# Kernel tuning notes

Hardware: AMD Instinct MI355X
Metric: run time of the kernel (lower is better)

Reference implementation:

```python
import jax, jax.numpy as jnp
import numpy as np

WINDOW = 2  # hardcoded global in the original module


def band_count(seq_len, window=WINDOW):
    """C[a,b] = number of positions i whose local window covers both a and b.
    Windows (from converse_qk): i=0 -> [0, W]; i=1 -> [0, W+1];
    i=seq-2 -> [seq-W-2, seq-1]; i=seq-1 -> [seq-W-1, seq-1]; else [i-W, i+W].
    """
    i = jnp.arange(seq_len)
    lo = jnp.clip(i - window, 0, None)
    hi = jnp.clip(i + window, None, seq_len - 1)
    lo = jnp.where(i == 1, 0, lo)
    hi = jnp.where(i == 1, window + 1, hi)
    lo = jnp.where(i == seq_len - 2, seq_len - window - 2, lo)
    hi = jnp.where(i == seq_len - 2, seq_len - 1, hi)
    a = jnp.arange(seq_len)[None, :]
    M = ((a >= lo[:, None]) & (a <= hi[:, None])).astype(jnp.float32)  # [i, a]
    return M.T @ M  # [seq, seq]


def setup_inputs() -> dict:
    key = jax.random.key(0)
    ks = jax.random.split(key, 12)
    bs, seq, d_model = 2, 2048, 512
    s = 1.0 / np.sqrt(d_model)
    inp = {
        'q': jax.random.normal(ks[0], (bs, seq, d_model), jnp.float32),
        'k': jax.random.normal(ks[1], (bs, seq, d_model), jnp.float32),
        'v': jax.random.normal(ks[2], (bs, seq, d_model), jnp.float32),
        'Wq': jax.random.normal(ks[3], (d_model, d_model), jnp.float32) * s,
        'bq': jnp.zeros((d_model,), jnp.float32),
        'Wk': jax.random.normal(ks[4], (d_model, d_model), jnp.float32) * s,
        'bk': jnp.zeros((d_model,), jnp.float32),
        'Wv': jax.random.normal(ks[5], (d_model, d_model), jnp.float32) * s,
        'bv': jnp.zeros((d_model,), jnp.float32),
        'Wo': jax.random.normal(ks[6], (d_model, d_model), jnp.float32) * s,
        'bo': jnp.zeros((d_model,), jnp.float32),
    }
    return inp


def reference(q, k, v, Wq, bq, Wk, bk, Wv, bv, Wo, bo):
    bs, seq, d_model = q.shape
    heads = 8
    d_k = d_model // heads
    # projections (torch Linear uses x @ W.T + b; here W stored already transposed)
    qh = (q @ Wq + bq).reshape(bs, seq, heads, d_k).transpose(0, 2, 1, 3)
    kh = (k @ Wk + bk).reshape(bs, seq, heads, d_k).transpose(0, 2, 1, 3)
    vh = (v @ Wv + bv).reshape(bs, seq, heads, d_k).transpose(0, 2, 1, 3)
    C = band_count(seq)  # [seq, seq] window-overlap counts
    scores = jnp.einsum('bhqd,bhkd->bhqk', qh, kh) / jnp.sqrt(jnp.float32(d_k))
    scores = scores * C  # banded count-weighted scores; zeros outside band
    attn = jax.nn.softmax(scores, axis=-1)  # full-row softmax, as in original
    out = jnp.einsum('bhqk,bhkd->bhqd', attn, vh)
    concat = out.transpose(0, 2, 1, 3).reshape(bs, seq, d_model)
    return concat @ Wo + bo
```

## Files before the change

kernel.cpp:

```cpp
#include <hip/hip_runtime.h>
#include <hip/hip_bf16.h>

#define SEQ 2048
#define DM  512
#define BS  2
#define NH  8
#define DK  64
#define MROWS (BS * SEQ)
#define GK 64

typedef __attribute__((ext_vector_type(8))) short bf16x8;
typedef __attribute__((ext_vector_type(4))) float f32x4;

__device__ __forceinline__ unsigned short f2bf(float f) {
    unsigned int u = __float_as_uint(f);
    u += 0x7fff + ((u >> 16) & 1);
    return (unsigned short)(u >> 16);
}
__device__ __forceinline__ float bf2f(unsigned short b) {
    return __uint_as_float((unsigned int)b << 16);
}

#define GLDS16(g, l) __builtin_amdgcn_global_load_lds( \
    (const __attribute__((address_space(1))) void*)(g), \
    (__attribute__((address_space(3))) void*)(unsigned int)(unsigned long long)(l), 16, 0, 0)

__global__ __launch_bounds__(256) void prep_w(const float* __restrict__ Wq, const float* __restrict__ Wk,
                                              const float* __restrict__ Wv, const float* __restrict__ Wo,
                                              const float* __restrict__ bv_,
                                              unsigned short* __restrict__ WqT, unsigned short* __restrict__ WkT,
                                              unsigned short* __restrict__ WvT, unsigned short* __restrict__ WoT,
                                              float* __restrict__ vsum)
{
    __shared__ float tile[32][33];
    const int bid = blockIdx.x;
    if (bid == 0) {
        #pragma unroll
        for (int t = 0; t < 4; ++t) {
            const int idx = threadIdx.x * 4 + t;
            vsum[idx] = (float)SEQ * bv_[idx & (DM - 1)];
        }
    }
    const int z = bid >> 8;
    const int tl = bid & 255;
    const float* W = (z == 0) ? Wq : (z == 1) ? Wk : (z == 2) ? Wv : Wo;
    unsigned short* T = (z == 0) ? WqT : (z == 1) ? WkT : (z == 2) ? WvT : WoT;
    const int n0 = (tl & 15) * 32, k0 = (tl >> 4) * 32;
    const int tx = threadIdx.x & 31;
    const int ty = threadIdx.x >> 5;
    #pragma unroll
    for (int r = 0; r < 32; r += 8)
        tile[ty + r][tx] = W[(size_t)(k0 + ty + r) * DM + n0 + tx];
    __syncthreads();
    #pragma unroll
    for (int r = 0; r < 32; r += 8)
        T[(size_t)(n0 + ty + r) * DM + k0 + tx] = f2bf(tile[tx][ty + r]);
}

__global__ __launch_bounds__(256) void gemm_qkv_cvt(const float* __restrict__ q,
                                                    const float* __restrict__ k,
                                                    const float* __restrict__ v,
                                                    const unsigned short* __restrict__ WqT,
                                                    const unsigned short* __restrict__ WkT,
                                                    const unsigned short* __restrict__ WvT,
                                                    const float* __restrict__ bq, const float* __restrict__ bk,
                                                    const float* __restrict__ bvp,
                                                    unsigned short* __restrict__ Qb, unsigned short* __restrict__ Kb,
                                                    unsigned short* __restrict__ Vb, float* __restrict__ vsum)
{
    __shared__ unsigned short S[2][12288];

    const int g = blockIdx.x;
    const int xcd   = g & 7;
    const int n_idx = (g >> 3) & 3;
    const int t_    = g >> 5;
    const int strip = t_ * 8 + xcd;
    const int z     = strip >> 6;
    const int m0    = (strip & 63) * 64;
    const int n0    = n_idx * 128;

    const float* Af; const unsigned short* BT; const float* bias; unsigned short* C; float* vs;
    if (z == 0)      { Af = q; BT = WqT; bias = bq; C = Qb; vs = nullptr; }
    else if (z == 1) { Af = k; BT = WkT; bias = bk; C = Kb; vs = nullptr; }
    else             { Af = v; BT = WvT; bias = bvp; C = Vb; vs = vsum; }

    const int tid  = threadIdx.x;
    const int lane = tid & 63;
    const int wave = tid >> 6;
    const int wm = (wave & 1) * 32;
    const int wn = (wave >> 1) * 64;
    const int l15 = lane & 15;
    const int q8  = (lane >> 4) * 8;

    f32x4 acc[2][4];
    #pragma unroll
    for (int i = 0; i < 2; ++i)
        #pragma unroll
        for (int j = 0; j < 4; ++j)
            acc[i][j] = (f32x4){0.f, 0.f, 0.f, 0.f};

    const int arow = tid >> 4;
    const int akl  = (tid & 15) * 4;
    const int awoff = ((akl >> 5) * 2048) + (akl & 31);
    const float* agp = Af + (size_t)(m0 + arow) * DM + akl;

    const unsigned short* gb[4];
    int lboff[4];
    #pragma unroll
    for (int it = 0; it < 4; ++it) {
        const int c = tid + it * 256;
        const int n  = (c >> 2) & 127;
        const int kk = c >> 9;
        gb[it] = BT + (size_t)(n0 + n) * DM + kk * 32 + (c & 3) * 8;
        lboff[it] = 4096 + c * 8;
    }

    {
        #pragma unroll
        for (int it = 0; it < 4; ++it)
            GLDS16(gb[it], &S[0][lboff[it]]);
        float4 av[4];
        #pragma unroll
        for (int p = 0; p < 4; ++p)
            av[p] = *(const float4*)(agp + (size_t)p * 16 * DM);
        #pragma unroll
        for (int p = 0; p < 4; ++p) {
            unsigned int u0, u1;
            asm("v_cvt_pk_bf16_f32 %0, %1, %2" : "=v"(u0) : "v"(av[p].x), "v"(av[p].y));
            asm("v_cvt_pk_bf16_f32 %0, %1, %2" : "=v"(u1) : "v"(av[p].z), "v"(av[p].w));
            uint2 o; o.x = u0; o.y = u1;
            *(uint2*)&S[0][awoff + (p * 16 + arow) * 32] = o;
        }
    }
    __syncthreads();

    for (int t = 0; t < 8; ++t) {
        const int cur = t & 1, nxt = cur ^ 1;
        const int k0n = (t + 1) * GK;
        float4 av[4];
        if (t < 7) {
            #pragma unroll
            for (int it = 0; it < 4; ++it)
                GLDS16(gb[it] + k0n, &S[nxt][lboff[it]]);
            #pragma unroll
            for (int p = 0; p < 4; ++p)
                av[p] = *(const float4*)(agp + (size_t)p * 16 * DM + k0n);
        }

        #pragma unroll
        for (int kk = 0; kk < 2; ++kk) {
            bf16x8 af[2], bfr[4];
            #pragma unroll
            for (int i = 0; i < 2; ++i)
                af[i] = *(const bf16x8*)&S[cur][kk * 2048 + (wm + i * 16 + l15) * 32 + q8];
            #pragma unroll
            for (int j = 0; j < 4; ++j)
                bfr[j] = *(const bf16x8*)&S[cur][4096 + kk * 4096 + (wn + j * 16 + l15) * 32 + q8];
            #pragma unroll
            for (int i = 0; i < 2; ++i)
                #pragma unroll
                for (int j = 0; j < 4; ++j)
                    acc[i][j] = __builtin_amdgcn_mfma_f32_16x16x32_bf16(af[i], bfr[j], acc[i][j], 0, 0, 0);
        }

        if (t < 7) {
            #pragma unroll
            for (int p = 0; p < 4; ++p) {
                unsigned int u0, u1;
                asm("v_cvt_pk_bf16_f32 %0, %1, %2" : "=v"(u0) : "v"(av[p].x), "v"(av[p].y));
                asm("v_cvt_pk_bf16_f32 %0, %1, %2" : "=v"(u1) : "v"(av[p].z), "v"(av[p].w));
                uint2 o; o.x = u0; o.y = u1;
                *(uint2*)&S[nxt][awoff + (p * 16 + arow) * 32] = o;
            }
        }
        __syncthreads();
    }

    #pragma unroll
    for (int j = 0; j < 4; ++j) {
        const int col = n0 + wn + j * 16 + l15;
        const float bv = bias[col];
        #pragma unroll
        for (int i = 0; i < 2; ++i) {
            const int rbase = m0 + wm + i * 16 + (lane >> 4) * 4;
            #pragma unroll
            for (int r = 0; r < 4; ++r)
                C[(size_t)(rbase + r) * DM + col] = f2bf(acc[i][j][r] + bv);
        }
    }

    if (vs) {
        const int b = m0 >> 11;
        #pragma unroll
        for (int j = 0; j < 4; ++j) {
            float part = 0.f;
            #pragma unroll
            for (int i = 0; i < 2; ++i)
                #pragma unroll
                for (int r = 0; r < 4; ++r)
                    part += acc[i][j][r];
            part += __shfl_xor(part, 16, 64);
            part += __shfl_xor(part, 32, 64);
            if ((lane >> 4) == 0)
                atomicAdd(&vs[b * DM + n0 + wn + j * 16 + l15], part);
        }
    }
}

__global__ __launch_bounds__(64) void attn_mfma(const unsigned short* __restrict__ Qb,
                                                const unsigned short* __restrict__ Kb,
                                                const unsigned short* __restrict__ Vb,
                                                const float* __restrict__ vsum,
                                                unsigned short* __restrict__ concat)
{
    __shared__ unsigned short Wlds[16 * 32];
    __shared__ unsigned short Vt[32 * 70];
    const int lane = threadIdx.x;
    const int l15  = lane & 15;
    const int quad = lane >> 4;
    const int bh = blockIdx.y;
    const int b = bh >> 3, h = bh & 7;
    const int q0 = blockIdx.x * 16;
    const size_t rowbase = (size_t)b * SEQ;
    const int dbase = h * DK;

    bf16x8 vv[4];
    #pragma unroll
    for (int p = 0; p < 4; ++p) {
        const int idx = p * 64 + lane;
        const int row = idx >> 3, c8 = idx & 7;
        int kr = q0 - 4 + row;
        kr = min(max(kr, 0), SEQ - 1);
        vv[p] = *(const bf16x8*)&Vb[(rowbase + kr) * DM + dbase + c8 * 8];
    }

    const unsigned short* qrow = Qb + (rowbase + q0 + l15) * DM + dbase + quad * 8;
    const bf16x8 aq0 = *(const bf16x8*)(qrow);
    const bf16x8 aq1 = *(const bf16x8*)(qrow + 32);

    f32x4 sc[2];
    #pragma unroll
    for (int t = 0; t < 2; ++t) {
        int kp = q0 - 4 + t * 16 + l15;
        kp = min(max(kp, 0), SEQ - 1);
        const unsigned short* krow = Kb + (rowbase + kp) * DM + dbase + quad * 8;
        const bf16x8 b0 = *(const bf16x8*)(krow);
        const bf16x8 b1 = *(const bf16x8*)(krow + 32);
        f32x4 z = (f32x4){0.f, 0.f, 0.f, 0.f};
        z = __builtin_amdgcn_mfma_f32_16x16x32_bf16(aq0, b0, z, 0, 0, 0);
        sc[t] = __builtin_amdgcn_mfma_f32_16x16x32_bf16(aq1, b1, z, 0, 0, 0);
    }

    float dsum[4] = {0.f, 0.f, 0.f, 0.f};
    #pragma unroll
    for (int t = 0; t < 2; ++t) {
        const int kpos = q0 - 4 + t * 16 + l15;
        #pragma unroll
        for (int r = 0; r < 4; ++r) {
            const int qq = q0 + quad * 4 + r;
            const int mn = min(qq, kpos), mx = qq + kpos - mn;
            const float cnt = (float)(min(mn + 2, SEQ - 1) - max(mx - 2, 0) + 1);
            const float cw = (kpos >= 0 && kpos < SEQ && (mx - mn) <= 4) ? cnt * 0.125f : 0.f;
            const float w = expf(sc[t][r] * cw) - 1.f;
            const unsigned short wb = f2bf(w);
            Wlds[(quad * 4 + r) * 32 + t * 16 + l15] = wb;
            dsum[r] += bf2f(wb);
        }
    }
    #pragma unroll
    for (int off = 1; off <= 8; off <<= 1)
        #pragma unroll
        for (int r = 0; r < 4; ++r)
            dsum[r] += __shfl_xor(dsum[r], off, 64);

    #pragma unroll
    for (int p = 0; p < 4; ++p) {
        const int idx = p * 64 + lane;
        const int row = idx >> 3, c8 = idx & 7;
        *(bf16x8*)&Vt[row * 70 + c8 * 8] = vv[p];
    }
    __syncthreads();

    const bf16x8 aw = *(const bf16x8*)&Wlds[l15 * 32 + quad * 8];

    #pragma unroll
    for (int nt = 0; nt < 4; ++nt) {
        const int dl = nt * 16 + l15;
        bf16x8 bv_;
        #pragma unroll
        for (int j = 0; j < 8; ++j)
            bv_[j] = (short)Vt[(quad * 8 + j) * 70 + dl];
        f32x4 z = (f32x4){0.f, 0.f, 0.f, 0.f};
        const f32x4 o = __builtin_amdgcn_mfma_f32_16x16x32_bf16(aw, bv_, z, 0, 0, 0);
        const float vs = vsum[b * DM + dbase + dl];
        #pragma unroll
        for (int r = 0; r < 4; ++r) {
            const float den = (float)SEQ + dsum[r];
            concat[(rowbase + q0 + quad * 4 + r) * DM + dbase + dl] = f2bf((vs + o[r]) / den);
        }
    }
}

__global__ __launch_bounds__(256) void gemm_out(const unsigned short* __restrict__ A,
                                                const unsigned short* __restrict__ BT,
                                                const float* __restrict__ bias,
                                                float* __restrict__ C)
{
    __shared__ unsigned short S[2][8192];

    const int g = blockIdx.x;
    const int xcd   = g & 7;
    const int n_idx = (g >> 3) & 7;
    const int m_idx = (g >> 6) * 8 + xcd;
    const int m0 = m_idx * 64, n0 = n_idx * 64;

    const int tid  = threadIdx.x;
    const int lane = tid & 63;
    const int wave = tid >> 6;
    const int wm = (wave & 1) * 32;
    const int wn = (wave >> 1) * 32;
    const int l15 = lane & 15;
    const int q8  = (lane >> 4) * 8;

    f32x4 acc[2][2];
    #pragma unroll
    for (int i = 0; i < 2; ++i)
        #pragma unroll
        for (int j = 0; j < 2; ++j)
            acc[i][j] = (f32x4){0.f, 0.f, 0.f, 0.f};

    const unsigned short* gp[4];
    int lpoff[4];
    #pragma unroll
    for (int it = 0; it < 4; ++it) {
        const int c = tid + it * 256;
        if (c < 512) {
            const int kk = c >> 8;
            const int cr = c & 255;
            gp[it] = A + (size_t)(m0 + (cr >> 2)) * DM + kk * 32 + (c & 3) * 8;
        } else {
            const int cb = c - 512;
            const int kk = cb >> 8;
            const int cr = cb & 255;
            gp[it] = BT + (size_t)(n0 + (cr >> 2)) * DM + kk * 32 + (cb & 3) * 8;
        }
        lpoff[it] = c * 8;
    }

    #pragma unroll
    for (int it = 0; it < 4; ++it)
        GLDS16(gp[it], &S[0][lpoff[it]]);
    __syncthreads();

    for (int t = 0; t < 8; ++t) {
        const int cur = t & 1, nxt = cur ^ 1;
        if (t < 7) {
            const int k0n = (t + 1) * GK;
            #pragma unroll
            for (int it = 0; it < 4; ++it)
                GLDS16(gp[it] + k0n, &S[nxt][lpoff[it]]);
        }

        #pragma unroll
        for (int kk = 0; kk < 2; ++kk) {
            bf16x8 af[2], bfr[2];
            #pragma unroll
            for (int i = 0; i < 2; ++i)
                af[i] = *(const bf16x8*)&S[cur][kk * 2048 + (wm + i * 16 + l15) * 32 + q8];
            #pragma unroll
            for (int j = 0; j < 2; ++j)
                bfr[j] = *(const bf16x8*)&S[cur][4096 + kk * 2048 + (wn + j * 16 + l15) * 32 + q8];
            #pragma unroll
            for (int i = 0; i < 2; ++i)
                #pragma unroll
                for (int j = 0; j < 2; ++j)
                    acc[i][j] = __builtin_amdgcn_mfma_f32_16x16x32_bf16(af[i], bfr[j], acc[i][j], 0, 0, 0);
        }
        __syncthreads();
    }

    #pragma unroll
    for (int j = 0; j < 2; ++j) {
        const int col = n0 + wn + j * 16 + l15;
        const float bov = bias[col];
        #pragma unroll
        for (int i = 0; i < 2; ++i) {
            const int rbase = m0 + wm + i * 16 + (lane >> 4) * 4;
            #pragma unroll
            for (int r = 0; r < 4; ++r)
                C[(size_t)(rbase + r) * DM + col] = acc[i][j][r] + bov;
        }
    }
}

extern "C" void kernel_launch(void* const* d_in, const int* in_sizes, int n_in,
                              void* d_out, int out_size, void* d_ws, size_t ws_size,
                              hipStream_t stream) {
    const float* q  = (const float*)d_in[0];
    const float* k  = (const float*)d_in[1];
    const float* v  = (const float*)d_in[2];
    const float* Wq = (const float*)d_in[3];
    const float* bq = (const float*)d_in[4];
    const float* Wk = (const float*)d_in[5];
    const float* bk = (const float*)d_in[6];
    const float* Wv = (const float*)d_in[7];
    const float* bv = (const float*)d_in[8];
    const float* Wo = (const float*)d_in[9];
    const float* bo = (const float*)d_in[10];

    const size_t NE = (size_t)MROWS * DM;

    float* vsum = (float*)d_ws;
    unsigned short* Qb     = (unsigned short*)(vsum + 1024);
    unsigned short* Kb     = Qb + NE;
    unsigned short* Vb     = Kb + NE;
    unsigned short* WqT    = Vb + NE;
    unsigned short* WkT    = WqT + DM * DM;
    unsigned short* WvT    = WkT + DM * DM;
    unsigned short* WoT    = WvT + DM * DM;
    unsigned short* concat = WoT + DM * DM;

    prep_w<<<1024, 256, 0, stream>>>(Wq, Wk, Wv, Wo, bv, WqT, WkT, WvT, WoT, vsum);

    gemm_qkv_cvt<<<768, 256, 0, stream>>>(q, k, v, WqT, WkT, WvT,
                                          bq, bk, bv, Qb, Kb, Vb, vsum);

    attn_mfma<<<dim3(SEQ / 16, BS * NH), 64, 0, stream>>>(Qb, Kb, Vb, vsum, concat);

    gemm_out<<<512, 256, 0, stream>>>(concat, WoT, bo, (float*)d_out);
}
```

Baseline: 113.5 us.

## Triple-buffer B tiles and register-prefetch A in output GEMM; swizzle attention blocks

After: 119.9 us. 5.6% more time.

```diff
diff --git a/kernel.cpp b/kernel.cpp
--- a/kernel.cpp
+++ b/kernel.cpp
@@ -24,6 +24,8 @@
 #define GLDS16(g, l) __builtin_amdgcn_global_load_lds( \
     (const __attribute__((address_space(1))) void*)(g), \
     (__attribute__((address_space(3))) void*)(unsigned int)(unsigned long long)(l), 16, 0, 0)
+
+#define WAITVM(N) asm volatile("s_waitcnt vmcnt(" #N ")" ::: "memory")
 
 __global__ __launch_bounds__(256) void prep_w(const float* __restrict__ Wq, const float* __restrict__ Wk,
                                               const float* __restrict__ Wv, const float* __restrict__ Wo,
@@ -218,9 +220,11 @@
     const int lane = threadIdx.x;
     const int l15  = lane & 15;
     const int quad = lane >> 4;
-    const int bh = blockIdx.y;
+    const int flat = blockIdx.y * (SEQ / 16) + blockIdx.x;
+    const int swz  = (flat & 7) * 256 + (flat >> 3);
+    const int bh = swz >> 7;
     const int b = bh >> 3, h = bh & 7;
-    const int q0 = blockIdx.x * 16;
+    const int q0 = (swz & 127) * 16;
     const size_t rowbase = (size_t)b * SEQ;
     const int dbase = h * DK;
 
@@ -261,7 +265,7 @@
             const int mn = min(qq, kpos), mx = qq + kpos - mn;
             const float cnt = (float)(min(mn + 2, SEQ - 1) - max(mx - 2, 0) + 1);
             const float cw = (kpos >= 0 && kpos < SEQ && (mx - mn) <= 4) ? cnt * 0.125f : 0.f;
-            const float w = expf(sc[t][r] * cw) - 1.f;
+            const float w = __expf(sc[t][r] * cw) - 1.f;
             const unsigned short wb = f2bf(w);
             Wlds[(quad * 4 + r) * 32 + t * 16 + l15] = wb;
             dsum[r] += bf2f(wb);
@@ -279,6 +283,12 @@
         const int row = idx >> 3, c8 = idx & 7;
         *(bf16x8*)&Vt[row * 70 + c8 * 8] = vv[p];
     }
+
+    float vs4[4];
+    #pragma unroll
+    for (int nt = 0; nt < 4; ++nt)
+        vs4[nt] = vsum[b * DM + dbase + nt * 16 + l15];
+
     __syncthreads();
 
     const bf16x8 aw = *(const bf16x8*)&Wlds[l15 * 32 + quad * 8];
@@ -292,11 +302,10 @@
             bv_[j] = (short)Vt[(quad * 8 + j) * 70 + dl];
         f32x4 z = (f32x4){0.f, 0.f, 0.f, 0.f};
         const f32x4 o = __builtin_amdgcn_mfma_f32_16x16x32_bf16(aw, bv_, z, 0, 0, 0);
-        const float vs = vsum[b * DM + dbase + dl];
         #pragma unroll
         for (int r = 0; r < 4; ++r) {
             const float den = (float)SEQ + dsum[r];
-            concat[(rowbase + q0 + quad * 4 + r) * DM + dbase + dl] = f2bf((vs + o[r]) / den);
+            concat[(rowbase + q0 + quad * 4 + r) * DM + dbase + dl] = f2bf((vs4[nt] + o[r]) / den);
         }
     }
 }
@@ -306,7 +315,7 @@
                                                 const float* __restrict__ bias,
                                                 float* __restrict__ C)
 {
-    __shared__ unsigned short S[2][8192];
+    __shared__ unsigned short S[3][4096];
 
     const int g = blockIdx.x;
     const int xcd   = g & 7;
@@ -329,54 +338,76 @@
         for (int j = 0; j < 2; ++j)
             acc[i][j] = (f32x4){0.f, 0.f, 0.f, 0.f};
 
-    const unsigned short* gp[4];
-    int lpoff[4];
-    #pragma unroll
-    for (int it = 0; it < 4; ++it) {
+    const unsigned short* gp[2];
+    int lpoff[2];
+    #pragma unroll
+    for (int it = 0; it < 2; ++it) {
         const int c = tid + it * 256;
-        if (c < 512) {
-            const int kk = c >> 8;
-            const int cr = c & 255;
-            gp[it] = A + (size_t)(m0 + (cr >> 2)) * DM + kk * 32 + (c & 3) * 8;
-        } else {
-            const int cb = c - 512;
-            const int kk = cb >> 8;
-            const int cr = cb & 255;
-            gp[it] = BT + (size_t)(n0 + (cr >> 2)) * DM + kk * 32 + (cb & 3) * 8;
-        }
+        const int kk = c >> 8;
+        const int cr = c & 255;
+        gp[it] = BT + (size_t)(n0 + (cr >> 2)) * DM + kk * 32 + (c & 3) * 8;
         lpoff[it] = c * 8;
     }
 
-    #pragma unroll
-    for (int it = 0; it < 4; ++it)
+    const unsigned short* ap[2];
+    #pragma unroll
+    for (int i = 0; i < 2; ++i)
+        ap[i] = A + (size_t)(m0 + wm + i * 16 + l15) * DM + q8;
+
+    bf16x8 afc[2][2], afn[2][2];
+
+    #pragma unroll
+    for (int i = 0; i < 2; ++i)
+        #pragma unroll
+        for (int kk = 0; kk < 2; ++kk)
+            afc[i][kk] = *(const bf16x8*)(ap[i] + kk * 32);
+    #pragma unroll
+    for (int it = 0; it < 2; ++it)
         GLDS16(gp[it], &S[0][lpoff[it]]);
-    __syncthreads();
-
+    #pragma unroll
+    for (int it = 0; it < 2; ++it)
+        GLDS16(gp[it] + GK, &S[1][lpoff[it]]);
+    WAITVM(2);
+    __builtin_amdgcn_s_barrier();
+
+    #pragma unroll
     for (int t = 0; t < 8; ++t) {
-        const int cur = t & 1, nxt = cur ^ 1;
         if (t < 7) {
-            const int k0n = (t + 1) * GK;
-            #pragma unroll
-            for (int it = 0; it < 4; ++it)
-                GLDS16(gp[it] + k0n, &S[nxt][lpoff[it]]);
+            #pragma unroll
+            for (int i = 0; i < 2; ++i)
+                #pragma unroll
+                for (int kk = 0; kk < 2; ++kk)
+                    afn[i][kk] = *(const bf16x8*)(ap[i] + (t + 1) * GK + kk * 32);
+        }
+        if (t < 6) {
+            #pragma unroll
+            for (int it = 0; it < 2; ++it)
+                GLDS16(gp[it] + (t + 2) * GK, &S[(t + 2) % 3][lpoff[it]]);
         }
 
         #pragma unroll
         for (int kk = 0; kk < 2; ++kk) {
-            bf16x8 af[2], bfr[2];
-            #pragma unroll
-            for (int i = 0; i < 2; ++i)
-                af[i] = *(const bf16x8*)&S[cur][kk * 2048 + (wm + i * 16 + l15) * 32 + q8];
+            bf16x8 bfr[2];
             #pragma unroll
             for (int j = 0; j < 2; ++j)
-                bfr[j] = *(const bf16x8*)&S[cur][4096 + kk * 2048 + (wn + j * 16 + l15) * 32 + q8];
+                bfr[j] = *(const bf16x8*)&S[t % 3][kk * 2048 + (wn + j * 16 + l15) * 32 + q8];
             #pragma unroll
             for (int i = 0; i < 2; ++i)
                 #pragma unroll
                 for (int j = 0; j < 2; ++j)
-                    acc[i][j] = __builtin_amdgcn_mfma_f32_16x16x32_bf16(af[i], bfr[j], acc[i][j], 0, 0, 0);
-        }
-        __syncthreads();
+                    acc[i][j] = __builtin_amdgcn_mfma_f32_16x16x32_bf16(afc[i][kk], bfr[j], acc[i][j], 0, 0, 0);
+        }
+
+        if (t < 6)      { WAITVM(2); }
+        else if (t == 6){ WAITVM(4); }
+        if (t < 7) {
+            __builtin_amdgcn_s_barrier();
+            #pragma unroll
+            for (int i = 0; i < 2; ++i)
+                #pragma unroll
+                for (int kk = 0; kk < 2; ++kk)
+                    afc[i][kk] = afn[i][kk];
+        }
     }
 
     #pragma unroll
```
